# Kernel optimization log

Measured on AMD Instinct MI355X. Metric: run time of the kernel, lower is better.

Reference implementation:

```python
import jax, jax.numpy as jnp
import numpy as np

EPS = 1e-20


def setup_inputs() -> dict:
    key = jax.random.key(0)
    k_u, k_w = jax.random.split(key)
    B, n_in, d_in, N, D = 128, 1152, 8, 32, 16
    u = jax.random.normal(k_u, (B, n_in, d_in), dtype=jnp.float32)
    # xavier_normal for W: fan_in = d_in, fan_out = D (last two dims)
    std = float(np.sqrt(2.0 / (d_in + D)))
    W = jax.random.normal(k_w, (n_in, N, d_in, D), dtype=jnp.float32) * std
    b = jnp.zeros((n_in, N), dtype=jnp.float32)
    return {"u": u, "W": W, "b": b}


def reference(u, W, b):
    # u: [B, i, n]; W: [i, j, n, m]; u_hat: [B, i, j, m]
    u_hat = jnp.einsum('ijnm,bin->bijm', W, u)
    # agreement score uses detached (stop-gradient) u_hat
    u_hat_d = jax.lax.stop_gradient(u_hat)
    D = W.shape[-1]
    a = jnp.einsum('bijm,bijm->bij', u_hat_d, u_hat_d) / jnp.sqrt(jnp.float32(D))
    # softmax over parent-capsule axis j, plus learned bias b[i, j]
    c = jax.nn.softmax(a, axis=2) + b[None, :, :]
    s = jnp.einsum('bij,bijm->bjm', c, u_hat)
    # squash nonlinearity
    n = jnp.linalg.norm(s, axis=-1, keepdims=True)
    v = (n * n / (1.0 + n * n) / (n + EPS)) * s
    return v
```

## Files before the change

### kernel.cpp

```cpp
#include <hip/hip_runtime.h>
#include <math.h>


#define NB 128
#define NI 1152
#define NJ 32
#define DM 16
#define JMSZ 512
#define BB 4

__device__ __forceinline__ float4 ldsW(const float* base, int j, int byteInRow) {
  int byte = (j << 9) + byteInRow;
  byte ^= ((j & 7) << 4);
  return *(const float4*)((const char*)base + byte);
}

template <int TPB_>
__device__ __forceinline__ void stageW(float* dst, const float* src, int tid) {
#pragma unroll
  for (int q = 0; q < 1024 / TPB_; ++q) {
    int o = (tid + q * TPB_) << 4;
    int so = o ^ (((o >> 9) & 7) << 4);
    *(float4*)((char*)dst + so) = *(const float4*)((const char*)src + o);
  }
}

template <int TPB_, int IC_, bool ATOMIC>
__global__ __launch_bounds__(TPB_, 4) void caps_main(
    const float* __restrict__ u, const float* __restrict__ W,
    const float* __restrict__ bias, float* __restrict__ out, int nchunk) {
  __shared__ __align__(16) float wl[2][4096];
  constexpr int BPB_ = (TPB_ / 64) * BB;

  const int chunk = blockIdx.x;
  const int bg = blockIdx.y;
  const int tid = threadIdx.x;
  const int wid = tid >> 6;
  const int lane = tid & 63;
  const int j = lane >> 1;
  const int h = lane & 1;
  const int b0 = __builtin_amdgcn_readfirstlane(bg * BPB_ + wid * BB);
  const int i0 = chunk * IC_;

  stageW<TPB_>(wl[0], W + (size_t)i0 * 4096, tid);

  float acc[BB][8];
#pragma unroll
  for (int bb = 0; bb < BB; ++bb)
#pragma unroll
    for (int k = 0; k < 8; ++k) acc[bb][k] = 0.f;

  for (int t = 0; t < IC_; ++t) {
    const int i = i0 + t;
    __syncthreads();
    if (t + 1 < IC_) stageW<TPB_>(wl[(t + 1) & 1], W + (size_t)(i + 1) * 4096, tid);
    const float* wb = wl[t & 1];

    float un[BB][8];
#pragma unroll
    for (int bb = 0; bb < BB; ++bb) {
      const float* up = u + ((size_t)(b0 + bb) * NI + i) * 8;
      float4 a0 = *(const float4*)up;
      float4 a1 = *(const float4*)(up + 4);
      un[bb][0] = a0.x; un[bb][1] = a0.y; un[bb][2] = a0.z; un[bb][3] = a0.w;
      un[bb][4] = a1.x; un[bb][5] = a1.y; un[bb][6] = a1.z; un[bb][7] = a1.w;
    }
    const float bj = bias[(size_t)i * NJ + j];

    float uh[BB][8];
#pragma unroll
    for (int bb = 0; bb < BB; ++bb)
#pragma unroll
      for (int k = 0; k < 8; ++k) uh[bb][k] = 0.f;

#pragma unroll
    for (int n = 0; n < 8; ++n) {
      const int rb = n * 64 + h * 32;
      float4 w0 = ldsW(wb, j, rb);
      float4 w1 = ldsW(wb, j, rb + 16);
#pragma unroll
      for (int bb = 0; bb < BB; ++bb) {
        const float uv = un[bb][n];
        uh[bb][0] = fmaf(uv, w0.x, uh[bb][0]);
        uh[bb][1] = fmaf(uv, w0.y, uh[bb][1]);
        uh[bb][2] = fmaf(uv, w0.z, uh[bb][2]);
        uh[bb][3] = fmaf(uv, w0.w, uh[bb][3]);
        uh[bb][4] = fmaf(uv, w1.x, uh[bb][4]);
        uh[bb][5] = fmaf(uv, w1.y, uh[bb][5]);
        uh[bb][6] = fmaf(uv, w1.z, uh[bb][6]);
        uh[bb][7] = fmaf(uv, w1.w, uh[bb][7]);
      }
    }

#pragma unroll
    for (int bb = 0; bb < BB; ++bb) {
      float s2 = uh[bb][0] * uh[bb][0] + uh[bb][1] * uh[bb][1] +
                 uh[bb][2] * uh[bb][2] + uh[bb][3] * uh[bb][3] +
                 uh[bb][4] * uh[bb][4] + uh[bb][5] * uh[bb][5] +
                 uh[bb][6] * uh[bb][6] + uh[bb][7] * uh[bb][7];
      s2 += __shfl_xor(s2, 1);
      const float e = __expf(s2 * 0.25f);
      float es = e;
      es += __shfl_xor(es, 2);
      es += __shfl_xor(es, 4);
      es += __shfl_xor(es, 8);
      es += __shfl_xor(es, 16);
      es += __shfl_xor(es, 32);
      const float c = e * __builtin_amdgcn_rcpf(es) + bj;
#pragma unroll
      for (int k = 0; k < 8; ++k) acc[bb][k] = fmaf(c, uh[bb][k], acc[bb][k]);
    }
  }

#pragma unroll
  for (int bb = 0; bb < BB; ++bb) {
    if (ATOMIC) {
      float* p = out + (size_t)(b0 + bb) * JMSZ + j * DM + h * 8;
#pragma unroll
      for (int k = 0; k < 8; ++k) atomicAdd(p + k, acc[bb][k]);
    } else {
      float* p = out + ((size_t)(b0 + bb) * nchunk + chunk) * JMSZ + j * DM + h * 8;
      *(float4*)p = make_float4(acc[bb][0], acc[bb][1], acc[bb][2], acc[bb][3]);
      *(float4*)(p + 4) = make_float4(acc[bb][4], acc[bb][5], acc[bb][6], acc[bb][7]);
    }
  }
}

template <int NSUM>
__global__ __launch_bounds__(256) void caps_fin(const float* __restrict__ part,
                                                float* __restrict__ v) {
  const int gid = blockIdx.x * 256 + threadIdx.x;
  const int o = gid >> 2;
  const int q = gid & 3;
  float s;
  if constexpr (NSUM == 1) {
    s = part[o];
  } else {
    constexpr int QC = NSUM / 4;
    const int b = o >> 9;
    const int jm = o & 511;
    const float* p = part + (size_t)b * NSUM * JMSZ + (size_t)(q * QC) * JMSZ + jm;
    s = 0.f;
#pragma unroll
    for (int cc = 0; cc < QC; ++cc) s += p[(size_t)cc * JMSZ];
    s += __shfl_xor(s, 1);
    s += __shfl_xor(s, 2);
  }
  float sq = s * s;
  sq += __shfl_xor(sq, 4);
  sq += __shfl_xor(sq, 8);
  sq += __shfl_xor(sq, 16);
  sq += __shfl_xor(sq, 32);
  const float nrm = sqrtf(sq);
  const float f = (sq / (1.0f + sq)) / (nrm + 1e-20f);
  if (q == 0) v[o] = f * s;
}

extern "C" void kernel_launch(void* const* d_in, const int* in_sizes, int n_in,
                              void* d_out, int out_size, void* d_ws, size_t ws_size,
                              hipStream_t stream) {
  const float* u = (const float*)d_in[0];
  const float* W = (const float*)d_in[1];
  const float* bias = (const float*)d_in[2];
  float* out = (float*)d_out;

  const size_t P128 = (size_t)NB * 128 * JMSZ * sizeof(float);
  const size_t P64 = (size_t)NB * 64 * JMSZ * sizeof(float);
  const int finGrid = (NB * JMSZ * 4) / 256;

  if (ws_size >= P128) {
    float* part = (float*)d_ws;
    caps_main<256, 9, false><<<dim3(128, NB / 16), 256, 0, stream>>>(u, W, bias, part, 128);
    caps_fin<128><<<finGrid, 256, 0, stream>>>(part, out);
  } else if (ws_size >= P64) {
    float* part = (float*)d_ws;
    caps_main<256, 18, false><<<dim3(64, NB / 16), 256, 0, stream>>>(u, W, bias, part, 64);
    caps_fin<64><<<finGrid, 256, 0, stream>>>(part, out);
  } else {
    float* sbuf = (float*)d_ws;
    hipMemsetAsync(sbuf, 0, (size_t)NB * JMSZ * sizeof(float), stream);
    caps_main<256, 18, true><<<dim3(64, NB / 16), 256, 0, stream>>>(u, W, bias, sbuf, 64);
    caps_fin<1><<<finGrid, 256, 0, stream>>>(sbuf, out);
  }
}
```

Baseline: 104.5 us.

## Stage W via global_load_lds, split into more chunks, vectorize final reduction

```diff
diff --git a/kernel.cpp b/kernel.cpp
--- a/kernel.cpp
+++ b/kernel.cpp
@@ -8,6 +8,7 @@
 #define DM 16
 #define JMSZ 512
 #define BB 4
+#define TPB 256
 
 __device__ __forceinline__ float4 ldsW(const float* base, int j, int byteInRow) {
   int byte = (j << 9) + byteInRow;
@@ -15,45 +16,48 @@
   return *(const float4*)((const char*)base + byte);
 }
 
-template <int TPB_>
-__device__ __forceinline__ void stageW(float* dst, const float* src, int tid) {
-#pragma unroll
-  for (int q = 0; q < 1024 / TPB_; ++q) {
-    int o = (tid + q * TPB_) << 4;
-    int so = o ^ (((o >> 9) & 7) << 4);
-    *(float4*)((char*)dst + so) = *(const float4*)((const char*)src + o);
-  }
-}
-
-template <int TPB_, int IC_, bool ATOMIC>
-__global__ __launch_bounds__(TPB_, 4) void caps_main(
+__device__ __forceinline__ void stageW(float* dstLds, const float* src,
+                                       int wid, int lane) {
+#pragma unroll
+  for (int q = 0; q < 4; ++q) {
+    const int xbase = (q * 256 + wid * 64) * 16;
+    const int x = xbase + lane * 16;
+    const int so = x ^ (((x >> 9) & 7) << 4);
+    __builtin_amdgcn_global_load_lds((const char*)src + so,
+                                     (char*)dstLds + xbase, 16, 0, 0);
+  }
+}
+
+template <int IC_, bool ATOMIC>
+__global__ __launch_bounds__(TPB, 5) void caps_main(
     const float* __restrict__ u, const float* __restrict__ W,
     const float* __restrict__ bias, float* __restrict__ out, int nchunk) {
   __shared__ __align__(16) float wl[2][4096];
-  constexpr int BPB_ = (TPB_ / 64) * BB;
+  constexpr int BPB_ = (TPB / 64) * BB;
 
   const int chunk = blockIdx.x;
   const int bg = blockIdx.y;
   const int tid = threadIdx.x;
-  const int wid = tid >> 6;
+  const int wid = __builtin_amdgcn_readfirstlane(tid >> 6);
   const int lane = tid & 63;
   const int j = lane >> 1;
   const int h = lane & 1;
   const int b0 = __builtin_amdgcn_readfirstlane(bg * BPB_ + wid * BB);
   const int i0 = chunk * IC_;
 
-  stageW<TPB_>(wl[0], W + (size_t)i0 * 4096, tid);
+  stageW(wl[0], W + (size_t)i0 * 4096, wid, lane);
 
   float acc[BB][8];
 #pragma unroll
   for (int bb = 0; bb < BB; ++bb)
 #pragma unroll
     for (int k = 0; k < 8; ++k) acc[bb][k] = 0.f;
+
+  __syncthreads();
 
   for (int t = 0; t < IC_; ++t) {
     const int i = i0 + t;
-    __syncthreads();
-    if (t + 1 < IC_) stageW<TPB_>(wl[(t + 1) & 1], W + (size_t)(i + 1) * 4096, tid);
+    if (t + 1 < IC_) stageW(wl[(t + 1) & 1], W + (size_t)(i + 1) * 4096, wid, lane);
     const float* wb = wl[t & 1];
 
     float un[BB][8];
@@ -110,6 +114,8 @@
 #pragma unroll
       for (int k = 0; k < 8; ++k) acc[bb][k] = fmaf(c, uh[bb][k], acc[bb][k]);
     }
+
+    __syncthreads();
   }
 
 #pragma unroll
@@ -129,31 +135,47 @@
 template <int NSUM>
 __global__ __launch_bounds__(256) void caps_fin(const float* __restrict__ part,
                                                 float* __restrict__ v) {
-  const int gid = blockIdx.x * 256 + threadIdx.x;
-  const int o = gid >> 2;
-  const int q = gid & 3;
-  float s;
   if constexpr (NSUM == 1) {
-    s = part[o];
+    const int o = blockIdx.x * 256 + threadIdx.x;
+    const float s = part[o];
+    float sq = s * s;
+    sq += __shfl_xor(sq, 1);
+    sq += __shfl_xor(sq, 2);
+    sq += __shfl_xor(sq, 4);
+    sq += __shfl_xor(sq, 8);
+    const float nrm = sqrtf(sq);
+    v[o] = (sq / (1.0f + sq)) / (nrm + 1e-20f) * s;
   } else {
-    constexpr int QC = NSUM / 4;
-    const int b = o >> 9;
-    const int jm = o & 511;
-    const float* p = part + (size_t)b * NSUM * JMSZ + (size_t)(q * QC) * JMSZ + jm;
-    s = 0.f;
-#pragma unroll
-    for (int cc = 0; cc < QC; ++cc) s += p[(size_t)cc * JMSZ];
-    s += __shfl_xor(s, 1);
-    s += __shfl_xor(s, 2);
-  }
-  float sq = s * s;
-  sq += __shfl_xor(sq, 4);
-  sq += __shfl_xor(sq, 8);
-  sq += __shfl_xor(sq, 16);
-  sq += __shfl_xor(sq, 32);
-  const float nrm = sqrtf(sq);
-  const float f = (sq / (1.0f + sq)) / (nrm + 1e-20f);
-  if (q == 0) v[o] = f * s;
+    constexpr int QC = NSUM / 8;
+    const int lane = threadIdx.x & 63;
+    const int wv = (blockIdx.x * 256 + threadIdx.x) >> 6;
+    const int q = lane >> 3;
+    const int r = lane & 7;
+    const int F = wv * 8 + r;
+    const int b = F >> 7;
+    const int jm4 = F & 127;
+    const float* p = part + (size_t)b * NSUM * JMSZ + (size_t)q * QC * JMSZ + jm4 * 4;
+    float4 s4 = make_float4(0.f, 0.f, 0.f, 0.f);
+#pragma unroll 4
+    for (int cc = 0; cc < QC; ++cc) {
+      float4 x = *(const float4*)(p + (size_t)cc * JMSZ);
+      s4.x += x.x; s4.y += x.y; s4.z += x.z; s4.w += x.w;
+    }
+#pragma unroll
+    for (int mask = 8; mask <= 32; mask <<= 1) {
+      s4.x += __shfl_xor(s4.x, mask);
+      s4.y += __shfl_xor(s4.y, mask);
+      s4.z += __shfl_xor(s4.z, mask);
+      s4.w += __shfl_xor(s4.w, mask);
+    }
+    float sq = s4.x * s4.x + s4.y * s4.y + s4.z * s4.z + s4.w * s4.w;
+    sq += __shfl_xor(sq, 1);
+    sq += __shfl_xor(sq, 2);
+    const float nrm = sqrtf(sq);
+    const float f = (sq / (1.0f + sq)) / (nrm + 1e-20f);
+    if (q == 0)
+      *(float4*)(v + (size_t)F * 4) = make_float4(f * s4.x, f * s4.y, f * s4.z, f * s4.w);
+  }
 }
 
 extern "C" void kernel_launch(void* const* d_in, const int* in_sizes, int n_in,
@@ -164,22 +186,21 @@
   const float* bias = (const float*)d_in[2];
   float* out = (float*)d_out;
 
-  const size_t P128 = (size_t)NB * 128 * JMSZ * sizeof(float);
+  const size_t P192 = (size_t)NB * 192 * JMSZ * sizeof(float);
   const size_t P64 = (size_t)NB * 64 * JMSZ * sizeof(float);
-  const int finGrid = (NB * JMSZ * 4) / 256;
-
-  if (ws_size >= P128) {
+
+  if (ws_size >= P192) {
     float* part = (float*)d_ws;
-    caps_main<256, 9, false><<<dim3(128, NB / 16), 256, 0, stream>>>(u, W, bias, part, 128);
-    caps_fin<128><<<finGrid, 256, 0, stream>>>(part, out);
+    caps_main<6, false><<<dim3(192, 8), TPB, 0, stream>>>(u, W, bias, part, 192);
+    caps_fin<192><<<512, 256, 0, stream>>>(part, out);
   } else if (ws_size >= P64) {
     float* part = (float*)d_ws;
-    caps_main<256, 18, false><<<dim3(64, NB / 16), 256, 0, stream>>>(u, W, bias, part, 64);
-    caps_fin<64><<<finGrid, 256, 0, stream>>>(part, out);
+    caps_main<18, false><<<dim3(64, 8), TPB, 0, stream>>>(u, W, bias, part, 64);
+    caps_fin<64><<<512, 256, 0, stream>>>(part, out);
   } else {
     float* sbuf = (float*)d_ws;
     hipMemsetAsync(sbuf, 0, (size_t)NB * JMSZ * sizeof(float), stream);
-    caps_main<256, 18, true><<<dim3(64, NB / 16), 256, 0, stream>>>(u, W, bias, sbuf, 64);
-    caps_fin<1><<<finGrid, 256, 0, stream>>>(sbuf, out);
-  }
-}
+    caps_main<18, true><<<dim3(64, 8), TPB, 0, stream>>>(u, W, bias, sbuf, 64);
+    caps_fin<1><<<(NB * JMSZ) / 256, 256, 0, stream>>>(sbuf, out);
+  }
+}
```

Result: slower. 131.9 us (+26.1%).
